# Performance work log

Hardware: AMD Instinct MI355X
Metric: run time of the kernel (lower is better)

Reference implementation:

```python
import jax, jax.numpy as jnp
import numpy as np

B, S, D, UNITS = 64, 2048, 512, 256

def setup_inputs() -> dict:
    key = jax.random.key(0)
    ks = jax.random.split(key, 8)
    sd = 1.0 / np.sqrt(D)
    query = jax.random.normal(ks[0], (B, D), dtype=jnp.float32)
    values = jax.random.normal(ks[1], (B, S, D), dtype=jnp.float32)
    W1 = jax.random.normal(ks[2], (D, UNITS), dtype=jnp.float32) * sd
    b1 = jnp.zeros((UNITS,), dtype=jnp.float32)
    W2 = jax.random.normal(ks[3], (D, UNITS), dtype=jnp.float32) * sd
    b2 = jnp.zeros((UNITS,), dtype=jnp.float32)
    V = jax.random.normal(ks[4], (UNITS, 1), dtype=jnp.float32) * (1.0 / np.sqrt(UNITS))
    bV = jnp.zeros((1,), dtype=jnp.float32)
    return {"query": query, "values": values, "W1": W1, "b1": b1,
            "W2": W2, "b2": b2, "V": V, "bV": bV}

def reference(query, values, W1, b1, W2, b2, V, bV):
    # proj_v: [B, S, U]; proj_q: [B, 1, U]
    proj_v = jnp.einsum('bsd,du->bsu', values, W1) + b1
    proj_q = (query @ W2 + b2)[:, None, :]
    # score: [B, S, 1]
    score = jnp.tanh(proj_v + proj_q) @ V + bV
    attn = jax.nn.softmax(score, axis=1)           # softmax over sequence axis
    context = jnp.sum(attn * values, axis=1)        # [B, D]
    return context
```

## Files before the change

### kernel.cpp

```cpp
#include <hip/hip_runtime.h>
#include <hip/hip_bf16.h>

typedef unsigned short u16;
typedef unsigned int u32;
typedef __attribute__((ext_vector_type(8))) short short8;
typedef __attribute__((ext_vector_type(4))) float f32x4;

#define NB 64
#define NS 2048
#define ND 512
#define NU 256

__device__ __forceinline__ u16 f2b(float f) {
    u32 x = __float_as_uint(f);
    u32 r = (x + 0x7FFFu + ((x >> 16) & 1u)) >> 16;
    return (u16)r;
}
__device__ __forceinline__ u32 pk2(float lo, float hi) {
    __hip_bfloat162 h = __float22bfloat162_rn(float2{lo, hi});
    return *(u32*)&h;
}
__device__ __forceinline__ float fast_tanh(float x) {
    float e = __expf(2.0f * x);
    return 1.0f - 2.0f / (e + 1.0f);
}

__global__ __launch_bounds__(256) void cbias_kernel(
    const float* __restrict__ q, const float* __restrict__ W2,
    const float* __restrict__ b1, const float* __restrict__ b2,
    float* __restrict__ cb)
{
    int b = blockIdx.x, u = threadIdx.x;
    __shared__ float qs[ND];
    qs[u]       = q[b * ND + u];
    qs[u + 256] = q[b * ND + u + 256];
    __syncthreads();
    float acc = 0.f;
#pragma unroll 8
    for (int d = 0; d < ND; d++)
        acc += qs[d] * W2[d * NU + u];
    cb[b * NU + u] = acc + b1[u] + b2[u];
}

__global__ __launch_bounds__(256) void transpose_kernel(
    const float* __restrict__ W1, u16* __restrict__ W1Tc)
{
    __shared__ float tile[64][65];
    int k0 = blockIdx.x * 64;
    int u0 = blockIdx.y * 64;
    for (int i = threadIdx.x; i < 4096; i += 256) {
        int r = i >> 6, c = i & 63;
        tile[r][c] = W1[(k0 + r) * NU + u0 + c];
    }
    __syncthreads();
    for (int i = threadIdx.x; i < 4096; i += 256) {
        int r = i >> 6, c = i & 63;
        W1Tc[blockIdx.x * (NU * 64) + (u0 + r) * 64 + c] = f2b(tile[c][r]);
    }
}

__global__ __launch_bounds__(256, 3) void score_kernel(
    const float* __restrict__ values,
    const u16* __restrict__ W1Tc,
    const float* __restrict__ cb,
    const float* __restrict__ V,
    float* __restrict__ scores)
{
    const int tid  = threadIdx.x;
    const int lane = tid & 63;
    const int wn   = tid >> 6;
    const int m16  = lane & 15;
    const int quad = lane >> 4;

    const int mblk = blockIdx.x;
    const int b    = mblk >> 5;
    const size_t base_row = (size_t)mblk * 64;

    __shared__ u16 At[64][72];
    __shared__ u16 Bt[256][72];
    __shared__ float cbs[NU];
    __shared__ float Vs[NU];
    __shared__ float rowsum[64];

    cbs[tid] = cb[b * NU + tid];
    Vs[tid]  = V[tid];
    if (tid < 64) rowsum[tid] = 0.f;

    f32x4 acc[4][4] = {};

    const float* Abase = values + base_row * ND;
    const int arow = tid >> 2, aseg = tid & 3;

    for (int kc = 0; kc < 8; kc++) {
        const int k0 = kc * 64;
        {
            const float* src = Abase + (size_t)arow * ND + k0 + aseg * 16;
            float4 v0 = ((const float4*)src)[0];
            float4 v1 = ((const float4*)src)[1];
            float4 v2 = ((const float4*)src)[2];
            float4 v3 = ((const float4*)src)[3];
            uint4 q0, q1;
            q0.x = pk2(v0.x, v0.y); q0.y = pk2(v0.z, v0.w);
            q0.z = pk2(v1.x, v1.y); q0.w = pk2(v1.z, v1.w);
            q1.x = pk2(v2.x, v2.y); q1.y = pk2(v2.z, v2.w);
            q1.z = pk2(v3.x, v3.y); q1.w = pk2(v3.z, v3.w);
            *(uint4*)&At[arow][aseg * 16]     = q0;
            *(uint4*)&At[arow][aseg * 16 + 8] = q1;
        }
        {
            const uint4* bsrc = (const uint4*)(W1Tc + (size_t)kc * (NU * 64) + tid * 64);
#pragma unroll
            for (int j = 0; j < 8; j++)
                *(uint4*)&Bt[tid][j * 8] = bsrc[j];
        }
        __syncthreads();

#pragma unroll
        for (int kh = 0; kh < 2; kh++) {
            short8 afr[4], bfr[4];
#pragma unroll
            for (int rb = 0; rb < 4; rb++)
                afr[rb] = *(const short8*)&At[rb * 16 + m16][kh * 32 + quad * 8];
#pragma unroll
            for (int cbk = 0; cbk < 4; cbk++)
                bfr[cbk] = *(const short8*)&Bt[wn * 64 + cbk * 16 + m16][kh * 32 + quad * 8];
#pragma unroll
            for (int rb = 0; rb < 4; rb++)
#pragma unroll
                for (int cbk = 0; cbk < 4; cbk++)
                    acc[rb][cbk] = __builtin_amdgcn_mfma_f32_16x16x32_bf16(
                        afr[rb], bfr[cbk], acc[rb][cbk], 0, 0, 0);
        }
        __syncthreads();
    }

    float cbv[4], vv[4];
#pragma unroll
    for (int cbk = 0; cbk < 4; cbk++) {
        int c = wn * 64 + cbk * 16 + m16;
        cbv[cbk] = cbs[c];
        vv[cbk]  = Vs[c];
    }
#pragma unroll
    for (int rb = 0; rb < 4; rb++) {
#pragma unroll
        for (int i = 0; i < 4; i++) {
            float s = 0.f;
#pragma unroll
            for (int cbk = 0; cbk < 4; cbk++)
                s += fast_tanh(acc[rb][cbk][i] + cbv[cbk]) * vv[cbk];
            s += __shfl_xor(s, 1, 64);
            s += __shfl_xor(s, 2, 64);
            s += __shfl_xor(s, 4, 64);
            s += __shfl_xor(s, 8, 64);
            if (m16 == 0)
                atomicAdd(&rowsum[rb * 16 + quad * 4 + i], s);
        }
    }
    __syncthreads();
    if (tid < 64) scores[base_row + tid] = rowsum[tid];
}

__global__ __launch_bounds__(256) void softmax_kernel(
    const float* __restrict__ scores, float* __restrict__ attn)
{
    int b = blockIdx.x, tid = threadIdx.x;
    __shared__ float red[256];
    const float* s = scores + (size_t)b * NS;
    float v[8];
    float mx = -1e30f;
#pragma unroll
    for (int i = 0; i < 8; i++) { v[i] = s[tid + i * 256]; mx = fmaxf(mx, v[i]); }
    red[tid] = mx; __syncthreads();
    for (int off = 128; off > 0; off >>= 1) {
        if (tid < off) red[tid] = fmaxf(red[tid], red[tid + off]);
        __syncthreads();
    }
    mx = red[0]; __syncthreads();
    float sum = 0.f;
#pragma unroll
    for (int i = 0; i < 8; i++) { v[i] = __expf(v[i] - mx); sum += v[i]; }
    red[tid] = sum; __syncthreads();
    for (int off = 128; off > 0; off >>= 1) {
        if (tid < off) red[tid] += red[tid + off];
        __syncthreads();
    }
    float inv = 1.0f / red[0];
#pragma unroll
    for (int i = 0; i < 8; i++) attn[(size_t)b * NS + tid + i * 256] = v[i] * inv;
}

__global__ __launch_bounds__(256) void context_kernel(
    const float* __restrict__ values, const float* __restrict__ attn,
    float* __restrict__ partial)
{
    int sc = blockIdx.x, b = blockIdx.y, tid = threadIdx.x;
    int srow = tid >> 5;
    int dcol = tid & 31;
    __shared__ float at[64];
    __shared__ float part[8][ND];
    if (tid < 64) at[tid] = attn[(size_t)b * NS + sc * 64 + tid];
    __syncthreads();
    float acc[16] = {};
    const float* vb = values + ((size_t)b * NS + (size_t)sc * 64) * ND;
#pragma unroll 2
    for (int i = 0; i < 8; i++) {
        int sl = i * 8 + srow;
        float a = at[sl];
        const float* row = vb + (size_t)sl * ND + dcol * 4;
        float4 r0 = *(const float4*)(row);
        float4 r1 = *(const float4*)(row + 128);
        float4 r2 = *(const float4*)(row + 256);
        float4 r3 = *(const float4*)(row + 384);
        acc[0]  += a * r0.x; acc[1]  += a * r0.y; acc[2]  += a * r0.z; acc[3]  += a * r0.w;
        acc[4]  += a * r1.x; acc[5]  += a * r1.y; acc[6]  += a * r1.z; acc[7]  += a * r1.w;
        acc[8]  += a * r2.x; acc[9]  += a * r2.y; acc[10] += a * r2.z; acc[11] += a * r2.w;
        acc[12] += a * r3.x; acc[13] += a * r3.y; acc[14] += a * r3.z; acc[15] += a * r3.w;
    }
#pragma unroll
    for (int j = 0; j < 4; j++)
        *(float4*)&part[srow][j * 128 + dcol * 4] =
            float4{acc[j*4], acc[j*4+1], acc[j*4+2], acc[j*4+3]};
    __syncthreads();
    for (int d = tid; d < ND; d += 256) {
        float s = 0.f;
#pragma unroll
        for (int r = 0; r < 8; r++) s += part[r][d];
        partial[((size_t)b * 32 + sc) * ND + d] = s;
    }
}

__global__ __launch_bounds__(256) void finalize_kernel(
    const float* __restrict__ partial, float* __restrict__ out)
{
    int idx = blockIdx.x * 256 + threadIdx.x;
    int b = idx >> 9, d = idx & 511;
    float s = 0.f;
#pragma unroll
    for (int sc = 0; sc < 32; sc++)
        s += partial[((size_t)b * 32 + sc) * ND + d];
    out[idx] = s;
}

extern "C" void kernel_launch(void* const* d_in, const int* in_sizes, int n_in,
                              void* d_out, int out_size, void* d_ws, size_t ws_size,
                              hipStream_t stream)
{
    const float* q      = (const float*)d_in[0];
    const float* values = (const float*)d_in[1];
    const float* W1     = (const float*)d_in[2];
    const float* b1     = (const float*)d_in[3];
    const float* W2     = (const float*)d_in[4];
    const float* b2     = (const float*)d_in[5];
    const float* V      = (const float*)d_in[6];

    char* ws = (char*)d_ws;
    float* cb      = (float*)(ws);
    u16*   W1Tc    = (u16*)  (ws + 65536);
    float* scores  = (float*)(ws + 327680);
    float* attn    = (float*)(ws + 851968);
    float* partial = (float*)(ws + 1376256);

    hipLaunchKernelGGL(cbias_kernel, dim3(64), dim3(256), 0, stream, q, W2, b1, b2, cb);
    hipLaunchKernelGGL(transpose_kernel, dim3(8, 4), dim3(256), 0, stream, W1, W1Tc);
    hipLaunchKernelGGL(score_kernel, dim3(2048), dim3(256), 0, stream,
                       values, W1Tc, cb, V, scores);
    hipLaunchKernelGGL(softmax_kernel, dim3(64), dim3(256), 0, stream, scores, attn);
    hipLaunchKernelGGL(context_kernel, dim3(32, 64), dim3(256), 0, stream,
                       values, attn, partial);
    hipLaunchKernelGGL(finalize_kernel, dim3(128), dim3(256), 0, stream,
                       partial, (float*)d_out);
}
```

Measured before the change: 485.7 us.

## Fuse score, softmax and context into one kernel with split-softmax combine

```diff
diff --git a/kernel.cpp b/kernel.cpp
--- a/kernel.cpp
+++ b/kernel.cpp
@@ -10,6 +10,7 @@
 #define NS 2048
 #define ND 512
 #define NU 256
+#define ASTR 520
 
 __device__ __forceinline__ u16 f2b(float f) {
     u32 x = __float_as_uint(f);
@@ -59,12 +60,13 @@
     }
 }
 
-__global__ __launch_bounds__(256, 3) void score_kernel(
+__global__ __launch_bounds__(256, 2) void fused_kernel(
     const float* __restrict__ values,
     const u16* __restrict__ W1Tc,
     const float* __restrict__ cb,
     const float* __restrict__ V,
-    float* __restrict__ scores)
+    float* __restrict__ ctxp,
+    float2* __restrict__ meta)
 {
     const int tid  = threadIdx.x;
     const int lane = tid & 63;
@@ -76,11 +78,12 @@
     const int b    = mblk >> 5;
     const size_t base_row = (size_t)mblk * 64;
 
-    __shared__ u16 At[64][72];
-    __shared__ u16 Bt[256][72];
+    __shared__ u16 Afull[64][ASTR];
     __shared__ float cbs[NU];
     __shared__ float Vs[NU];
     __shared__ float rowsum[64];
+    __shared__ float wsm[64];
+    __shared__ float mred[2];
 
     cbs[tid] = cb[b * NU + tid];
     Vs[tid]  = V[tid];
@@ -88,48 +91,51 @@
 
     f32x4 acc[4][4] = {};
 
-    const float* Abase = values + base_row * ND;
-    const int arow = tid >> 2, aseg = tid & 3;
+    const float* asrc = values + (base_row + (tid >> 2)) * ND + (tid & 3) * 16;
+    const int arow = tid >> 2, acol = (tid & 3) * 16;
+
+    float4 v0 = ((const float4*)asrc)[0];
+    float4 v1 = ((const float4*)asrc)[1];
+    float4 v2 = ((const float4*)asrc)[2];
+    float4 v3 = ((const float4*)asrc)[3];
 
     for (int kc = 0; kc < 8; kc++) {
-        const int k0 = kc * 64;
         {
-            const float* src = Abase + (size_t)arow * ND + k0 + aseg * 16;
-            float4 v0 = ((const float4*)src)[0];
-            float4 v1 = ((const float4*)src)[1];
-            float4 v2 = ((const float4*)src)[2];
-            float4 v3 = ((const float4*)src)[3];
             uint4 q0, q1;
             q0.x = pk2(v0.x, v0.y); q0.y = pk2(v0.z, v0.w);
             q0.z = pk2(v1.x, v1.y); q0.w = pk2(v1.z, v1.w);
             q1.x = pk2(v2.x, v2.y); q1.y = pk2(v2.z, v2.w);
             q1.z = pk2(v3.x, v3.y); q1.w = pk2(v3.z, v3.w);
-            *(uint4*)&At[arow][aseg * 16]     = q0;
-            *(uint4*)&At[arow][aseg * 16 + 8] = q1;
-        }
-        {
-            const uint4* bsrc = (const uint4*)(W1Tc + (size_t)kc * (NU * 64) + tid * 64);
-#pragma unroll
-            for (int j = 0; j < 8; j++)
-                *(uint4*)&Bt[tid][j * 8] = bsrc[j];
+            *(uint4*)&Afull[arow][kc * 64 + acol]     = q0;
+            *(uint4*)&Afull[arow][kc * 64 + acol + 8] = q1;
         }
         __syncthreads();
-
+        if (kc < 7) {
+            const float* nsrc = asrc + (kc + 1) * 64;
+            v0 = ((const float4*)nsrc)[0];
+            v1 = ((const float4*)nsrc)[1];
+            v2 = ((const float4*)nsrc)[2];
+            v3 = ((const float4*)nsrc)[3];
+        }
+        short8 bfr[2][4];
+#pragma unroll
+        for (int kh = 0; kh < 2; kh++)
+#pragma unroll
+            for (int cbk = 0; cbk < 4; cbk++)
+                bfr[kh][cbk] = *(const short8*)(W1Tc + (size_t)kc * (NU * 64)
+                                + (wn * 64 + cbk * 16 + m16) * 64 + kh * 32 + quad * 8);
 #pragma unroll
         for (int kh = 0; kh < 2; kh++) {
-            short8 afr[4], bfr[4];
+            short8 afr[4];
 #pragma unroll
             for (int rb = 0; rb < 4; rb++)
-                afr[rb] = *(const short8*)&At[rb * 16 + m16][kh * 32 + quad * 8];
-#pragma unroll
-            for (int cbk = 0; cbk < 4; cbk++)
-                bfr[cbk] = *(const short8*)&Bt[wn * 64 + cbk * 16 + m16][kh * 32 + quad * 8];
+                afr[rb] = *(const short8*)&Afull[rb * 16 + m16][kc * 64 + kh * 32 + quad * 8];
 #pragma unroll
             for (int rb = 0; rb < 4; rb++)
 #pragma unroll
                 for (int cbk = 0; cbk < 4; cbk++)
                     acc[rb][cbk] = __builtin_amdgcn_mfma_f32_16x16x32_bf16(
-                        afr[rb], bfr[cbk], acc[rb][cbk], 0, 0, 0);
+                        afr[rb], bfr[kh][cbk], acc[rb][cbk], 0, 0, 0);
         }
         __syncthreads();
     }
@@ -158,88 +164,78 @@
         }
     }
     __syncthreads();
-    if (tid < 64) scores[base_row + tid] = rowsum[tid];
-}
-
-__global__ __launch_bounds__(256) void softmax_kernel(
-    const float* __restrict__ scores, float* __restrict__ attn)
+
+    if (tid < 64) {
+        float s = rowsum[tid];
+        float m = s;
+        m = fmaxf(m, __shfl_xor(m, 1, 64));
+        m = fmaxf(m, __shfl_xor(m, 2, 64));
+        m = fmaxf(m, __shfl_xor(m, 4, 64));
+        m = fmaxf(m, __shfl_xor(m, 8, 64));
+        m = fmaxf(m, __shfl_xor(m, 16, 64));
+        m = fmaxf(m, __shfl_xor(m, 32, 64));
+        float w = __expf(s - m);
+        wsm[tid] = w;
+        float l = w;
+        l += __shfl_xor(l, 1, 64);
+        l += __shfl_xor(l, 2, 64);
+        l += __shfl_xor(l, 4, 64);
+        l += __shfl_xor(l, 8, 64);
+        l += __shfl_xor(l, 16, 64);
+        l += __shfl_xor(l, 32, 64);
+        if (tid == 0) { mred[0] = m; mred[1] = l; }
+    }
+    __syncthreads();
+
+    {
+        const u32* adw = (const u32*)&Afull[0][0];
+        float a0 = 0.f, a1 = 0.f;
+#pragma unroll 8
+        for (int r = 0; r < 64; r++) {
+            u32 pk = adw[r * (ASTR / 2) + tid];
+            float lo = __uint_as_float(pk << 16);
+            float hi = __uint_as_float(pk & 0xFFFF0000u);
+            float wt = wsm[r];
+            a0 += wt * lo;
+            a1 += wt * hi;
+        }
+        float* dst = ctxp + (size_t)mblk * ND + tid * 2;
+        dst[0] = a0;
+        dst[1] = a1;
+    }
+    if (tid == 0) meta[mblk] = float2{mred[0], mred[1]};
+}
+
+__global__ __launch_bounds__(256) void combine_kernel(
+    const float* __restrict__ ctxp, const float2* __restrict__ meta,
+    float* __restrict__ out)
 {
     int b = blockIdx.x, tid = threadIdx.x;
-    __shared__ float red[256];
-    const float* s = scores + (size_t)b * NS;
-    float v[8];
-    float mx = -1e30f;
-#pragma unroll
-    for (int i = 0; i < 8; i++) { v[i] = s[tid + i * 256]; mx = fmaxf(mx, v[i]); }
-    red[tid] = mx; __syncthreads();
-    for (int off = 128; off > 0; off >>= 1) {
-        if (tid < off) red[tid] = fmaxf(red[tid], red[tid + off]);
-        __syncthreads();
-    }
-    mx = red[0]; __syncthreads();
-    float sum = 0.f;
-#pragma unroll
-    for (int i = 0; i < 8; i++) { v[i] = __expf(v[i] - mx); sum += v[i]; }
-    red[tid] = sum; __syncthreads();
-    for (int off = 128; off > 0; off >>= 1) {
-        if (tid < off) red[tid] += red[tid + off];
-        __syncthreads();
-    }
-    float inv = 1.0f / red[0];
-#pragma unroll
-    for (int i = 0; i < 8; i++) attn[(size_t)b * NS + tid + i * 256] = v[i] * inv;
-}
-
-__global__ __launch_bounds__(256) void context_kernel(
-    const float* __restrict__ values, const float* __restrict__ attn,
-    float* __restrict__ partial)
-{
-    int sc = blockIdx.x, b = blockIdx.y, tid = threadIdx.x;
-    int srow = tid >> 5;
-    int dcol = tid & 31;
-    __shared__ float at[64];
-    __shared__ float part[8][ND];
-    if (tid < 64) at[tid] = attn[(size_t)b * NS + sc * 64 + tid];
-    __syncthreads();
-    float acc[16] = {};
-    const float* vb = values + ((size_t)b * NS + (size_t)sc * 64) * ND;
-#pragma unroll 2
-    for (int i = 0; i < 8; i++) {
-        int sl = i * 8 + srow;
-        float a = at[sl];
-        const float* row = vb + (size_t)sl * ND + dcol * 4;
-        float4 r0 = *(const float4*)(row);
-        float4 r1 = *(const float4*)(row + 128);
-        float4 r2 = *(const float4*)(row + 256);
-        float4 r3 = *(const float4*)(row + 384);
-        acc[0]  += a * r0.x; acc[1]  += a * r0.y; acc[2]  += a * r0.z; acc[3]  += a * r0.w;
-        acc[4]  += a * r1.x; acc[5]  += a * r1.y; acc[6]  += a * r1.z; acc[7]  += a * r1.w;
-        acc[8]  += a * r2.x; acc[9]  += a * r2.y; acc[10] += a * r2.z; acc[11] += a * r2.w;
-        acc[12] += a * r3.x; acc[13] += a * r3.y; acc[14] += a * r3.z; acc[15] += a * r3.w;
-    }
-#pragma unroll
-    for (int j = 0; j < 4; j++)
-        *(float4*)&part[srow][j * 128 + dcol * 4] =
-            float4{acc[j*4], acc[j*4+1], acc[j*4+2], acc[j*4+3]};
-    __syncthreads();
-    for (int d = tid; d < ND; d += 256) {
-        float s = 0.f;
-#pragma unroll
-        for (int r = 0; r < 8; r++) s += part[r][d];
-        partial[((size_t)b * 32 + sc) * ND + d] = s;
-    }
-}
-
-__global__ __launch_bounds__(256) void finalize_kernel(
-    const float* __restrict__ partial, float* __restrict__ out)
-{
-    int idx = blockIdx.x * 256 + threadIdx.x;
-    int b = idx >> 9, d = idx & 511;
-    float s = 0.f;
-#pragma unroll
-    for (int sc = 0; sc < 32; sc++)
-        s += partial[((size_t)b * 32 + sc) * ND + d];
-    out[idx] = s;
+    __shared__ float wc[32];
+    __shared__ float Ls;
+    if (tid == 0) {
+        float M = -1e30f;
+        for (int c = 0; c < 32; c++) M = fmaxf(M, meta[b * 32 + c].x);
+        float L = 0.f;
+        for (int c = 0; c < 32; c++) {
+            float w = __expf(meta[b * 32 + c].x - M);
+            wc[c] = w;
+            L += w * meta[b * 32 + c].y;
+        }
+        Ls = L;
+    }
+    __syncthreads();
+    float inv = 1.0f / Ls;
+    float s0 = 0.f, s1 = 0.f;
+#pragma unroll 4
+    for (int c = 0; c < 32; c++) {
+        const float* p = ctxp + ((size_t)b * 32 + c) * ND;
+        float w = wc[c];
+        s0 += w * p[tid];
+        s1 += w * p[tid + 256];
+    }
+    out[b * ND + tid]       = s0 * inv;
+    out[b * ND + tid + 256] = s1 * inv;
 }
 
 extern "C" void kernel_launch(void* const* d_in, const int* in_sizes, int n_in,
@@ -255,19 +251,15 @@
     const float* V      = (const float*)d_in[6];
 
     char* ws = (char*)d_ws;
-    float* cb      = (float*)(ws);
-    u16*   W1Tc    = (u16*)  (ws + 65536);
-    float* scores  = (float*)(ws + 327680);
-    float* attn    = (float*)(ws + 851968);
-    float* partial = (float*)(ws + 1376256);
+    float*  cb    = (float*) (ws);
+    u16*    W1Tc  = (u16*)   (ws + 65536);
+    float*  ctxp  = (float*) (ws + 327680);
+    float2* meta  = (float2*)(ws + 327680 + 4194304);
 
     hipLaunchKernelGGL(cbias_kernel, dim3(64), dim3(256), 0, stream, q, W2, b1, b2, cb);
     hipLaunchKernelGGL(transpose_kernel, dim3(8, 4), dim3(256), 0, stream, W1, W1Tc);
-    hipLaunchKernelGGL(score_kernel, dim3(2048), dim3(256), 0, stream,
-                       values, W1Tc, cb, V, scores);
-    hipLaunchKernelGGL(softmax_kernel, dim3(64), dim3(256), 0, stream, scores, attn);
-    hipLaunchKernelGGL(context_kernel, dim3(32, 64), dim3(256), 0, stream,
-                       values, attn, partial);
-    hipLaunchKernelGGL(finalize_kernel, dim3(128), dim3(256), 0, stream,
-                       partial, (float*)d_out);
-}
+    hipLaunchKernelGGL(fused_kernel, dim3(2048), dim3(256), 0, stream,
+                       values, W1Tc, cb, V, ctxp, meta);
+    hipLaunchKernelGGL(combine_kernel, dim3(64), dim3(256), 0, stream,
+                       ctxp, meta, (float*)d_out);
+}
```

Result: faster. 463.0 us (-4.7%).
